# Kernel tuning notes

Measured on AMD Instinct MI355X. Metric: run time of the kernel, lower is better.

Reference implementation:

```python
import jax, jax.numpy as jnp
import numpy as np

T, B, D, H, O = 128, 256, 512, 1024, 1


def setup_inputs() -> dict:
    key = jax.random.key(0)
    ks = jax.random.split(key, 10)
    s_in = 1.0 / np.sqrt(D)
    s_h = 1.0 / np.sqrt(H)
    u = lambda k, shape, s: jax.random.uniform(k, shape, jnp.float32, -s, s)
    return {
        "inputs": jax.random.normal(ks[0], (T, B, D), jnp.float32),
        "hidden_state": jnp.zeros((1, B, H), jnp.float32),
        "cell_state": jnp.zeros((1, B, H), jnp.float32),
        "W1": u(ks[1], (H, D), s_in),
        "b1": u(ks[2], (H,), s_in),
        "W_ih": u(ks[3], (4 * H, H), s_h),
        "W_hh": u(ks[4], (4 * H, H), s_h),
        "b_ih": u(ks[5], (4 * H,), s_h),
        "b_hh": u(ks[6], (4 * H,), s_h),
        "W_out": u(ks[7], (O, H), s_h),
        "b_out": u(ks[8], (O,), s_h),
    }


def reference(inputs, hidden_state, cell_state, W1, b1, W_ih, W_hh, b_ih, b_hh, W_out, b_out):
    # first_layer + ReLU (dropout is identity in eval mode)
    x = jax.nn.relu(jnp.einsum("tbd,hd->tbh", inputs, W1) + b1)  # (T,B,H)
    # Precompute input contribution to all gates for every timestep.
    xg = jnp.einsum("tbh,gh->tbg", x, W_ih) + b_ih + b_hh  # (T,B,4H)
    h0 = hidden_state[0]
    c0 = cell_state[0]

    def step(carry, xg_t):
        h, c = carry
        g = xg_t + h @ W_hh.T  # (B,4H), PyTorch gate order i,f,g,o
        i, f, gg, o = jnp.split(g, 4, axis=-1)
        i = jax.nn.sigmoid(i)
        f = jax.nn.sigmoid(f)
        gg = jnp.tanh(gg)
        o = jax.nn.sigmoid(o)
        c = f * c + i * gg
        h = o * jnp.tanh(c)
        return (h, c), h

    (hT, cT), hs = jax.lax.scan(step, (h0, c0), xg)
    out = jnp.einsum("tbh,oh->tbo", hs, W_out) + b_out  # (T,B,O)
    return out, hT[None], cT[None]
```

## Files before the change

### kernel.cpp

```cpp
#include <hip/hip_runtime.h>
#include <hip/hip_bf16.h>
#include <math.h>


#define T_STEPS 128
#define BATCH   256
#define DIM     512
#define HID     1024
#define GATES   4096
#define FPAD    32

typedef __attribute__((ext_vector_type(8))) short short8;
typedef __attribute__((ext_vector_type(4))) float f4;
typedef __attribute__((ext_vector_type(4))) int i4;

__device__ __forceinline__ short f2bf(float f) {
    union { float f; unsigned u; } x; x.f = f;
    unsigned r = (x.u + 0x7fffu + ((x.u >> 16) & 1u)) >> 16;
    return (short)r;
}
__device__ __forceinline__ float bf2f(short s) {
    union { unsigned u; float f; } x; x.u = ((unsigned)(unsigned short)s) << 16;
    return x.f;
}
__device__ __forceinline__ float sigm(float x) { return 1.f / (1.f + __expf(-x)); }
__device__ __forceinline__ float tanh_fast(float x) { return 2.f / (1.f + __expf(-2.f * x)) - 1.f; }

__device__ __forceinline__ void gll16(const void* g, void* l) {
    __builtin_amdgcn_global_load_lds(
        (const __attribute__((address_space(1))) void*)g,
        (__attribute__((address_space(3))) void*)l, 16, 0, 0);
}
__device__ __forceinline__ void store16_wt(void* p, i4 v) {
    asm volatile("global_store_dwordx4 %0, %1, off sc0 sc1"
                 :: "v"(p), "v"(v) : "memory");
}

__global__ __launch_bounds__(256) void cvt_f32_bf16(const float* __restrict__ in,
                                                    short* __restrict__ out, int n4) {
    int i = blockIdx.x * 256 + threadIdx.x;
    if (i < n4) {
        float4 v = ((const float4*)in)[i];
        union { short s[4]; long long ll; } r;
        r.s[0] = f2bf(v.x); r.s[1] = f2bf(v.y); r.s[2] = f2bf(v.z); r.s[3] = f2bf(v.w);
        ((long long*)out)[i] = r.ll;
    }
}

__global__ __launch_bounds__(256) void cvt_h0_blocked(const float* __restrict__ h0,
                                                      short* __restrict__ dst) {
    int b = blockIdx.x, k0 = threadIdx.x * 4;
    float4 v = *(const float4*)&h0[(size_t)b * HID + k0];
    union { short s[4]; long long ll; } p;
    p.s[0] = f2bf(v.x); p.s[1] = f2bf(v.y); p.s[2] = f2bf(v.z); p.s[3] = f2bf(v.w);
    *(long long*)&dst[(k0 >> 3) * (BATCH * 8) + b * 8 + (k0 & 7)] = p.ll;
}

__global__ __launch_bounds__(256) void cvt_permute_rows(const float* __restrict__ in,
                                                        short* __restrict__ out) {
    int r = blockIdx.x;
    int hc = r >> 2, g = r & 3;
    const float* src = in + (size_t)(g * HID + hc) * HID;
    short* dst = out + (size_t)r * HID;
    int c = threadIdx.x * 4;
    float4 v = *(const float4*)&src[c];
    union { short s[4]; long long ll; } p;
    p.s[0] = f2bf(v.x); p.s[1] = f2bf(v.y); p.s[2] = f2bf(v.z); p.s[3] = f2bf(v.w);
    *(long long*)&dst[c] = p.ll;
}

__global__ __launch_bounds__(256) void bias_sum_perm(const float* __restrict__ a,
                                                     const float* __restrict__ b,
                                                     float* __restrict__ o) {
    int r = blockIdx.x * 256 + threadIdx.x;
    int hc = r >> 2, g = r & 3;
    int src = g * HID + hc;
    o[r] = a[src] + b[src];
}

__global__ __launch_bounds__(256) void copy_f32v4(const float* __restrict__ in,
                                                  float* __restrict__ out, int n4) {
    int i = blockIdx.x * 256 + threadIdx.x;
    if (i < n4) ((float4*)out)[i] = ((const float4*)in)[i];
}

__global__ __launch_bounds__(256) void zero_i32(int* __restrict__ p, int n) {
    for (int i = blockIdx.x * 256 + threadIdx.x; i < n; i += gridDim.x * 256)
        p[i] = 0;
}

__global__ __launch_bounds__(256) void gemm_bt(const short* __restrict__ A,
                                               const short* __restrict__ B,
                                               const float* __restrict__ bias,
                                               short* __restrict__ C,
                                               int M, int N, int K, int do_relu) {
    __shared__ __align__(16) short As[128 * 32];
    __shared__ __align__(16) short Bs[128 * 32];
    const int tid = threadIdx.x, wave = tid >> 6, lane = tid & 63;
    const int wm = (wave >> 1) * 64, wn = (wave & 1) * 64;
    const int bm = blockIdx.x * 128, bn = blockIdx.y * 128;
    const int sr = lane >> 2, sc = (lane & 3) * 8;

    f4 acc[4][4] = {};

    for (int k0 = 0; k0 < K; k0 += 32) {
        __syncthreads();
#pragma unroll
        for (int j = 0; j < 2; ++j) {
            int c = wave * 2 + j;
            gll16(&A[(size_t)(bm + c * 16 + sr) * K + k0 + sc], &As[c * 512]);
            gll16(&B[(size_t)(bn + c * 16 + sr) * K + k0 + sc], &Bs[c * 512]);
        }
        __syncthreads();
        short8 af[4], bfr[4];
#pragma unroll
        for (int i = 0; i < 4; ++i) {
            af[i]  = *(const short8*)&As[(wm + i * 16 + (lane & 15)) * 32 + (lane >> 4) * 8];
            bfr[i] = *(const short8*)&Bs[(wn + i * 16 + (lane & 15)) * 32 + (lane >> 4) * 8];
        }
#pragma unroll
        for (int i = 0; i < 4; ++i)
#pragma unroll
            for (int j = 0; j < 4; ++j)
                acc[i][j] = __builtin_amdgcn_mfma_f32_16x16x32_bf16(af[i], bfr[j], acc[i][j], 0, 0, 0);
    }

    const int lc = lane & 15, lr = (lane >> 4) * 4;
#pragma unroll
    for (int i = 0; i < 4; ++i) {
#pragma unroll
        for (int j = 0; j < 4; ++j) {
            int col = bn + wn + j * 16 + lc;
            float bv = bias[col];
#pragma unroll
            for (int r = 0; r < 4; ++r) {
                int row = bm + wm + i * 16 + lr + r;
                float v = acc[i][j][r] + bv;
                if (do_relu) v = fmaxf(v, 0.f);
                C[(size_t)row * N + col] = f2bf(v);
            }
        }
    }
}

__global__ __launch_bounds__(256) void lstm_persist(const short* __restrict__ Whh,
                                                    const short* __restrict__ xgc,
                                                    short* __restrict__ hist,
                                                    float* __restrict__ cf,
                                                    float* __restrict__ hT,
                                                    float* __restrict__ cT,
                                                    int* __restrict__ flags,
                                                    int* __restrict__ go,
                                                    int TC, int last) {
    __shared__ __align__(16) short Bf[32768];
    __shared__ __align__(16) short Ht[512];
    const int tid = threadIdx.x, w = tid >> 6, lane = tid & 63;
    const int bg = blockIdx.x >> 7, cg = blockIdx.x & 127;
    const int bb = bg * 64, hc0 = cg * 8;
    const int hcl = lane & 7, gp = (lane >> 3) & 1, q = lane >> 4;

#pragma unroll
    for (int i = 0; i < 16; ++i) {
        int p = w * 16 + i;
        int c = p >> 1, t = p & 1;
        gll16(&Whh[(size_t)((t * 2 + gp) * HID + hc0 + hcl) * HID + c * 32 + q * 8],
              &Bf[p * 512]);
    }

    const int rowb = bb + w * 16 + q * 4 + gp * 2;
    float creg[2];
#pragma unroll
    for (int e = 0; e < 2; ++e)
        creg[e] = cf[(size_t)(rowb + e) * HID + hc0 + hcl];

    __syncthreads();

    unsigned long long xw[2], xwn[2];
#pragma unroll
    for (int e = 0; e < 2; ++e)
        xw[e] = *(const unsigned long long*)&xgc[(size_t)(rowb + e) * GATES
                                                 + (hc0 + hcl) * 4];

#define ISSUE_A(buf, g)                                                        \
    _Pragma("unroll")                                                          \
    for (int i = 0; i < 8; ++i)                                                \
        buf[i] = *(const short8*)(abase + (size_t)((g) * 8 + i) * astr);

#define COMPUTE_A(buf, g)                                                      \
    __builtin_amdgcn_s_setprio(1);                                             \
    _Pragma("unroll")                                                          \
    for (int i = 0; i < 8; ++i) {                                              \
        short8 b0 = *(const short8*)&Bf[(((g) * 8 + i) * 2 + 0) * 512 + lane * 8]; \
        short8 b1 = *(const short8*)&Bf[(((g) * 8 + i) * 2 + 1) * 512 + lane * 8]; \
        acc0 = __builtin_amdgcn_mfma_f32_16x16x32_bf16(buf[i], b0, acc0, 0, 0, 0); \
        acc1 = __builtin_amdgcn_mfma_f32_16x16x32_bf16(buf[i], b1, acc1, 0, 0, 0); \
    }                                                                          \
    __builtin_amdgcn_s_setprio(0);

    for (int tt = 0; tt < TC; ++tt) {
        if (tt + 1 < TC) {
#pragma unroll
            for (int e = 0; e < 2; ++e)
                xwn[e] = *(const unsigned long long*)&xgc[(size_t)((tt + 1) * BATCH + rowb + e) * GATES
                                                          + (hc0 + hcl) * 4];
        }

        const short* abase = hist + (size_t)tt * BATCH * HID
                           + (size_t)q * (BATCH * 8) + (size_t)(bb + w * 16 + (lane & 15)) * 8;
        const size_t astr = (size_t)4 * (BATCH * 8);
        f4 acc0 = {}, acc1 = {};
        short8 ab0[8], ab1[8], ab2[8];
        ISSUE_A(ab0, 0)
        ISSUE_A(ab1, 1)
        ISSUE_A(ab2, 2)
        COMPUTE_A(ab0, 0)
        ISSUE_A(ab0, 3)
        COMPUTE_A(ab1, 1)
        COMPUTE_A(ab2, 2)
        COMPUTE_A(ab0, 3)

        float p0[4], p1[4];
#pragma unroll
        for (int r = 0; r < 4; ++r) {
            p0[r] = __shfl_xor(acc0[r], 8);
            p1[r] = __shfl_xor(acc1[r], 8);
        }

        int glast = last && (tt == TC - 1);
#pragma unroll
        for (int e = 0; e < 2; ++e) {
            int r = gp * 2 + e;
            size_t b = rowb + e;
            float gi = gp ? p0[r] : acc0[r];
            float gf = gp ? acc0[r] : p0[r];
            float gg = gp ? p1[r] : acc1[r];
            float go_ = gp ? acc1[r] : p1[r];
            gi += bf2f((short)(xw[e] & 0xffff));
            gf += bf2f((short)((xw[e] >> 16) & 0xffff));
            gg += bf2f((short)((xw[e] >> 32) & 0xffff));
            go_ += bf2f((short)((xw[e] >> 48) & 0xffff));
            float si = sigm(gi), sf = sigm(gf), tg = tanh_fast(gg), so = sigm(go_);
            float cn = sf * creg[e] + si * tg;
            float hv = so * tanh_fast(cn);
            creg[e] = cn;
            Ht[(w * 16 + q * 4 + gp * 2 + e) * 8 + hcl] = f2bf(hv);
            if (glast) {
                hT[b * HID + hc0 + hcl] = hv;
                cT[b * HID + hc0 + hcl] = cn;
            }
        }
        xw[0] = xwn[0]; xw[1] = xwn[1];
        __syncthreads();

        short* hn = hist + (size_t)(tt + 1) * BATCH * HID
                  + (size_t)cg * (BATCH * 8) + (size_t)bb * 8;
        if (tid < 64)
            store16_wt(&hn[tid * 8], *(const i4*)&Ht[tid * 8]);

        if (tt < TC - 1) {
            __syncthreads();
            const int base = (tt * 4 + bg) * 128 * FPAD;
            if (tid == 0)
                __hip_atomic_store(&flags[base + cg * FPAD], 1,
                                   __ATOMIC_RELAXED, __HIP_MEMORY_SCOPE_AGENT);
            if (cg == 0) {
                if (tid < 128) {
                    while (__hip_atomic_load(&flags[base + tid * FPAD],
                                             __ATOMIC_RELAXED, __HIP_MEMORY_SCOPE_AGENT) == 0)
                        __builtin_amdgcn_s_sleep(1);
                }
                __syncthreads();
                if (tid == 0)
                    __hip_atomic_store(&go[(tt * 4 + bg) * FPAD], 1,
                                       __ATOMIC_RELAXED, __HIP_MEMORY_SCOPE_AGENT);
            } else {
                if (tid == 0) {
                    while (__hip_atomic_load(&go[(tt * 4 + bg) * FPAD],
                                             __ATOMIC_RELAXED, __HIP_MEMORY_SCOPE_AGENT) == 0)
                        __builtin_amdgcn_s_sleep(1);
                }
                __syncthreads();
            }
        }
    }

#undef ISSUE_A
#undef COMPUTE_A

#pragma unroll
    for (int e = 0; e < 2; ++e)
        cf[(size_t)(rowb + e) * HID + hc0 + hcl] = creg[e];
}

__global__ __launch_bounds__(256) void out_head(const short* __restrict__ hs,
                                                const float* __restrict__ Wout,
                                                const float* __restrict__ bout,
                                                float* __restrict__ out) {
    int row = blockIdx.x * 4 + (threadIdx.x >> 6);
    int lane = threadIdx.x & 63;
    int tt = row >> 8, b = row & 255;
    const short* sb = hs + (size_t)(tt + 1) * BATCH * HID + b * 8;
    const float2* w2 = (const float2*)Wout;
    float s = 0.f;
#pragma unroll
    for (int j = 0; j < 8; ++j) {
        int m = j * 64 + lane;
        int pk = *(const int*)&sb[(size_t)(m >> 2) * (BATCH * 8) + 2 * (m & 3)];
        float2 wv = w2[m];
        union { unsigned u; float f; } lo, hi;
        lo.u = ((unsigned)pk) << 16;
        hi.u = ((unsigned)pk) & 0xffff0000u;
        s += lo.f * wv.x + hi.f * wv.y;
    }
#pragma unroll
    for (int off = 32; off; off >>= 1) s += __shfl_down(s, off);
    if (lane == 0) out[row] = s + bout[0];
}

extern "C" void kernel_launch(void* const* d_in, const int* in_sizes, int n_in,
                              void* d_out, int out_size, void* d_ws, size_t ws_size,
                              hipStream_t stream) {
    const float* inputs = (const float*)d_in[0];
    const float* h0     = (const float*)d_in[1];
    const float* c0     = (const float*)d_in[2];
    const float* W1     = (const float*)d_in[3];
    const float* b1     = (const float*)d_in[4];
    const float* W_ih   = (const float*)d_in[5];
    const float* W_hh   = (const float*)d_in[6];
    const float* b_ih   = (const float*)d_in[7];
    const float* b_hh   = (const float*)d_in[8];
    const float* W_out  = (const float*)d_in[9];
    const float* b_out  = (const float*)d_in[10];

    float* out = (float*)d_out;
    float* hT  = out + (size_t)T_STEPS * BATCH;
    float* cT  = hT + (size_t)BATCH * HID;

    char* base = (char*)d_ws;
    size_t off = 0;
    auto alloc = [&](size_t bytes) -> char* {
        char* q = base + off;
        off += (bytes + 255) & ~(size_t)255;
        return q;
    };
    short* W1b   = (short*)alloc((size_t)HID * DIM * 2);
    short* Wihb  = (short*)alloc((size_t)GATES * HID * 2);
    short* Whhb  = (short*)alloc((size_t)GATES * HID * 2);
    float* biasf = (float*)alloc((size_t)GATES * 4);
    float* cf    = (float*)alloc((size_t)BATCH * HID * 4);
    int*   flags = (int*)alloc((size_t)T_STEPS * 4 * 128 * FPAD * 4);
    int*   go    = (int*)alloc((size_t)T_STEPS * 4 * FPAD * 4);

    size_t per_t = (size_t)BATCH * (DIM + HID + GATES) * 2 + (size_t)BATCH * HID * 2;
    int TC = 32;
    while (TC > 1 && off + (size_t)TC * per_t + (size_t)BATCH * HID * 2 + 65536 > ws_size)
        TC >>= 1;

    short* hhist = (short*)alloc((size_t)(TC + 1) * BATCH * HID * 2);
    short* inb_c = (short*)alloc((size_t)TC * BATCH * DIM * 2);
    short* xb_c  = (short*)alloc((size_t)TC * BATCH * HID * 2);
    short* xgb_c = (short*)alloc((size_t)TC * BATCH * GATES * 2);

    cvt_f32_bf16<<<(HID * DIM / 4 + 255) / 256, 256, 0, stream>>>(W1, W1b, HID * DIM / 4);
    cvt_permute_rows<<<GATES, 256, 0, stream>>>(W_ih, Wihb);
    cvt_f32_bf16<<<(GATES * HID / 4 + 255) / 256, 256, 0, stream>>>(W_hh, Whhb, GATES * HID / 4);
    bias_sum_perm<<<GATES / 256, 256, 0, stream>>>(b_ih, b_hh, biasf);
    cvt_h0_blocked<<<BATCH, 256, 0, stream>>>(h0, hhist);
    copy_f32v4<<<(BATCH * HID / 4 + 255) / 256, 256, 0, stream>>>(c0, cf, BATCH * HID / 4);
    zero_i32<<<512, 256, 0, stream>>>(flags, T_STEPS * 4 * 128 * FPAD + T_STEPS * 4 * FPAD);

    for (int t0 = 0; t0 < T_STEPS; t0 += TC) {
        int Mc = TC * BATCH;
        int last = (t0 + TC >= T_STEPS);
        cvt_f32_bf16<<<(Mc * DIM / 4 + 255) / 256, 256, 0, stream>>>(
            inputs + (size_t)t0 * BATCH * DIM, inb_c, Mc * DIM / 4);
        gemm_bt<<<dim3(Mc / 128, HID / 128), 256, 0, stream>>>(
            inb_c, W1b, b1, xb_c, Mc, HID, DIM, 1);
        gemm_bt<<<dim3(Mc / 128, GATES / 128), 256, 0, stream>>>(
            xb_c, Wihb, biasf, xgb_c, Mc, GATES, HID, 0);

        lstm_persist<<<512, 256, 0, stream>>>(Whhb, xgb_c, hhist, cf, hT, cT,
                                              flags + (size_t)t0 * 4 * 128 * FPAD,
                                              go + (size_t)t0 * 4 * FPAD,
                                              TC, last);

        out_head<<<TC * BATCH / 4, 256, 0, stream>>>(hhist, W_out, b_out,
                                                     out + (size_t)t0 * BATCH);
        copy_f32v4<<<(BATCH * HID * 2 / 16 + 255) / 256, 256, 0, stream>>>(
            (const float*)(hhist + (size_t)TC * BATCH * HID), (float*)hhist,
            BATCH * HID * 2 / 16);
    }
}
```

Before: 1.279 ms.

## Replace centralized per-step barrier with fine-grained per-chunk flag waits

Removes the two-level barrier, in which block cg==0 gathered all 128 flags and then raised a go flag. Instead, each block's wave 0 polls the producer flags for each group of 32 column blocks just before loading that group's slice of h, and signals the other waves through shared memory. Each group's loads and MFMAs can then start as soon as its own producers are done, which cuts out one round trip of global atomics and allows overlap with late producers. In exchange, every block now polls global flags, which adds polling traffic, and it relies on relaxed atomics for memory ordering.

```diff
diff --git a/kernel.cpp b/kernel.cpp
--- a/kernel.cpp
+++ b/kernel.cpp
@@ -150,14 +150,16 @@
                                                     float* __restrict__ hT,
                                                     float* __restrict__ cT,
                                                     int* __restrict__ flags,
-                                                    int* __restrict__ go,
                                                     int TC, int last) {
     __shared__ __align__(16) short Bf[32768];
     __shared__ __align__(16) short Ht[512];
+    __shared__ int rdy[4];
     const int tid = threadIdx.x, w = tid >> 6, lane = tid & 63;
     const int bg = blockIdx.x >> 7, cg = blockIdx.x & 127;
     const int bb = bg * 64, hc0 = cg * 8;
     const int hcl = lane & 7, gp = (lane >> 3) & 1, q = lane >> 4;
+
+    if (tid < 4) rdy[tid] = 0;
 
 #pragma unroll
     for (int i = 0; i < 16; ++i) {
@@ -180,6 +182,25 @@
     for (int e = 0; e < 2; ++e)
         xw[e] = *(const unsigned long long*)&xgc[(size_t)(rowb + e) * GATES
                                                  + (hc0 + hcl) * 4];
+
+#define WAIT_G(g)                                                              \
+    if (tt > 0) {                                                              \
+        if (w == 0) {                                                          \
+            if (lane < 32) {                                                   \
+                const int* fp = &flags[fb + ((g) * 32 + lane) * FPAD];         \
+                while (__hip_atomic_load(fp, __ATOMIC_RELAXED,                 \
+                                         __HIP_MEMORY_SCOPE_AGENT) == 0)       \
+                    __builtin_amdgcn_s_sleep(2);                               \
+            }                                                                  \
+            __hip_atomic_store(&rdy[g], tt, __ATOMIC_RELAXED,                  \
+                               __HIP_MEMORY_SCOPE_WORKGROUP);                  \
+        } else {                                                               \
+            while (__hip_atomic_load(&rdy[g], __ATOMIC_RELAXED,                \
+                                     __HIP_MEMORY_SCOPE_WORKGROUP) < tt)       \
+                __builtin_amdgcn_s_sleep(1);                                   \
+        }                                                                      \
+        __builtin_amdgcn_sched_barrier(0);                                     \
+    }
 
 #define ISSUE_A(buf, g)                                                        \
     _Pragma("unroll")                                                          \
@@ -205,15 +226,20 @@
                                                           + (hc0 + hcl) * 4];
         }
 
+        const int fb = ((tt - 1) * 4 + bg) * 128 * FPAD;
         const short* abase = hist + (size_t)tt * BATCH * HID
                            + (size_t)q * (BATCH * 8) + (size_t)(bb + w * 16 + (lane & 15)) * 8;
         const size_t astr = (size_t)4 * (BATCH * 8);
         f4 acc0 = {}, acc1 = {};
         short8 ab0[8], ab1[8], ab2[8];
+        WAIT_G(0)
         ISSUE_A(ab0, 0)
+        WAIT_G(1)
         ISSUE_A(ab1, 1)
+        WAIT_G(2)
         ISSUE_A(ab2, 2)
         COMPUTE_A(ab0, 0)
+        WAIT_G(3)
         ISSUE_A(ab0, 3)
         COMPUTE_A(ab1, 1)
         COMPUTE_A(ab2, 2)
@@ -259,31 +285,13 @@
 
         if (tt < TC - 1) {
             __syncthreads();
-            const int base = (tt * 4 + bg) * 128 * FPAD;
             if (tid == 0)
-                __hip_atomic_store(&flags[base + cg * FPAD], 1,
+                __hip_atomic_store(&flags[(tt * 4 + bg) * 128 * FPAD + cg * FPAD], 1,
                                    __ATOMIC_RELAXED, __HIP_MEMORY_SCOPE_AGENT);
-            if (cg == 0) {
-                if (tid < 128) {
-                    while (__hip_atomic_load(&flags[base + tid * FPAD],
-                                             __ATOMIC_RELAXED, __HIP_MEMORY_SCOPE_AGENT) == 0)
-                        __builtin_amdgcn_s_sleep(1);
-                }
-                __syncthreads();
-                if (tid == 0)
-                    __hip_atomic_store(&go[(tt * 4 + bg) * FPAD], 1,
-                                       __ATOMIC_RELAXED, __HIP_MEMORY_SCOPE_AGENT);
-            } else {
-                if (tid == 0) {
-                    while (__hip_atomic_load(&go[(tt * 4 + bg) * FPAD],
-                                             __ATOMIC_RELAXED, __HIP_MEMORY_SCOPE_AGENT) == 0)
-                        __builtin_amdgcn_s_sleep(1);
-                }
-                __syncthreads();
-            }
-        }
-    }
-
+        }
+    }
+
+#undef WAIT_G
 #undef ISSUE_A
 #undef COMPUTE_A
 
@@ -349,7 +357,6 @@
     float* biasf = (float*)alloc((size_t)GATES * 4);
     float* cf    = (float*)alloc((size_t)BATCH * HID * 4);
     int*   flags = (int*)alloc((size_t)T_STEPS * 4 * 128 * FPAD * 4);
-    int*   go    = (int*)alloc((size_t)T_STEPS * 4 * FPAD * 4);
 
     size_t per_t = (size_t)BATCH * (DIM + HID + GATES) * 2 + (size_t)BATCH * HID * 2;
     int TC = 32;
@@ -367,7 +374,7 @@
     bias_sum_perm<<<GATES / 256, 256, 0, stream>>>(b_ih, b_hh, biasf);
     cvt_h0_blocked<<<BATCH, 256, 0, stream>>>(h0, hhist);
     copy_f32v4<<<(BATCH * HID / 4 + 255) / 256, 256, 0, stream>>>(c0, cf, BATCH * HID / 4);
-    zero_i32<<<512, 256, 0, stream>>>(flags, T_STEPS * 4 * 128 * FPAD + T_STEPS * 4 * FPAD);
+    zero_i32<<<512, 256, 0, stream>>>(flags, T_STEPS * 4 * 128 * FPAD);
 
     for (int t0 = 0; t0 < T_STEPS; t0 += TC) {
         int Mc = TC * BATCH;
@@ -381,7 +388,6 @@
 
         lstm_persist<<<512, 256, 0, stream>>>(Whhb, xgb_c, hhist, cf, hT, cT,
                                               flags + (size_t)t0 * 4 * 128 * FPAD,
-                                              go + (size_t)t0 * 4 * FPAD,
                                               TC, last);
 
         out_head<<<TC * BATCH / 4, 256, 0, stream>>>(hhist, W_out, b_out,
```

Result: slower. 1.360 ms (+6.3%).
